# Performance work log

Hardware: AMD Instinct MI355X
Metric: run time of the kernel (lower is better)

## Reference

```python
import jax, jax.numpy as jnp
import numpy as np

N_NODES = 100000
N_EDGES = 250000
N_GRAPHS = 512
VOCAB = 1000
EMBED = 256
HIDDEN = 512
OUT = 128
EPS = 1e-5


def setup_inputs() -> dict:
    key = jax.random.key(0)
    ks = jax.random.split(key, 16)
    s = 0.02
    return {
        "x": jax.random.randint(ks[0], (N_NODES, 1), 0, VOCAB),
        "edge_index": jax.random.randint(ks[1], (2, N_EDGES), 0, N_NODES),
        "batch": jnp.sort(jax.random.randint(ks[2], (N_NODES,), 0, N_GRAPHS)),
        "emb": jax.random.normal(ks[3], (VOCAB, EMBED), jnp.float32) * s,
        "W1": jax.random.normal(ks[4], (EMBED, HIDDEN), jnp.float32) * s,
        "b1": jnp.zeros((HIDDEN,), jnp.float32),
        "g1": jnp.ones((HIDDEN,), jnp.float32),
        "be1": jnp.zeros((HIDDEN,), jnp.float32),
        "W2": jax.random.normal(ks[5], (HIDDEN, HIDDEN), jnp.float32) * s,
        "b2": jnp.zeros((HIDDEN,), jnp.float32),
        "g2": jnp.ones((HIDDEN,), jnp.float32),
        "be2": jnp.zeros((HIDDEN,), jnp.float32),
        "Wl1": jax.random.normal(ks[6], (HIDDEN, HIDDEN // 2), jnp.float32) * s,
        "bl1": jnp.zeros((HIDDEN // 2,), jnp.float32),
        "Wl2": jax.random.normal(ks[7], (HIDDEN // 2, OUT), jnp.float32) * s,
        "bl2": jnp.zeros((OUT,), jnp.float32),
    }


def _mpnn(h, edge_index, W, b):
    # sum-aggregate messages x_j from source to target, plus self-loop, then linear
    src, dst = edge_index[0], edge_index[1]
    agg = jax.ops.segment_sum(h[src], dst, num_segments=h.shape[0]) + h
    return agg @ W + b


def _bn(h, g, be):
    # BatchNorm1d, training-mode batch statistics (biased variance)
    mu = jnp.mean(h, axis=0)
    var = jnp.mean(jnp.square(h - mu), axis=0)
    return (h - mu) * jax.lax.rsqrt(var + EPS) * g + be


def reference(x, edge_index, batch, emb, W1, b1, g1, be1, W2, b2, g2, be2, Wl1, bl1, Wl2, bl2):
    h = emb[x[:, 0]]                                   # [N, EMBED]
    h = jax.nn.relu(_bn(_mpnn(h, edge_index, W1, b1), g1, be1))
    h = jax.nn.relu(_bn(_mpnn(h, edge_index, W2, b2), g2, be2))
    # global mean pool per graph
    sums = jax.ops.segment_sum(h, batch, num_segments=N_GRAPHS)
    cnts = jax.ops.segment_sum(jnp.ones((h.shape[0],), h.dtype), batch, num_segments=N_GRAPHS)
    pooled = sums / jnp.maximum(cnts, 1.0)[:, None]    # [G, HIDDEN]
    z = jax.nn.relu(pooled @ Wl1 + bl1)                # dropout is identity in eval
    return z @ Wl2 + bl2                               # [G, OUT]
```

## Files before the change

kernel.cpp:

```cpp
#include <hip/hip_runtime.h>
#include <cstdint>
#include <cstddef>

#define N_NODES 100000
#define N_EDGES 250000
#define N_GRAPHS 512
#define MTILES 782
#define MPAD (MTILES * 128)
#define SB 256
#define NBLK ((N_NODES + SB - 1) / SB)

using f32x4  = __attribute__((ext_vector_type(4))) float;
using bf16x8 = __attribute__((ext_vector_type(8))) short;

struct alignas(8) U16x4 { unsigned short x, y, z, w; };

__device__ __forceinline__ unsigned short f32_to_bf16(float f) {
    union { float f; uint32_t u; } v; v.f = f;
    uint32_t r = v.u + 0x7FFF + ((v.u >> 16) & 1);
    return (unsigned short)(r >> 16);
}
__device__ __forceinline__ float bf_lo(uint32_t u) {
    union { uint32_t u; float f; } v; v.u = u << 16; return v.f;
}
__device__ __forceinline__ float bf_hi(uint32_t u) {
    union { uint32_t u; float f; } v; v.u = u & 0xFFFF0000u; return v.f;
}

__device__ __forceinline__ void async_cp16(const void* g, void* l) {
    __builtin_amdgcn_global_load_lds(
        (const __attribute__((address_space(1))) void*)g,
        (__attribute__((address_space(3))) void*)l, 16, 0, 0);
}

__global__ void k_zero_int(int* __restrict__ p, int n) {
    int i = blockIdx.x * 256 + threadIdx.x;
    if (i < n) p[i] = 0;
}
__global__ void k_zero_f(float* __restrict__ p, int n) {
    int i = blockIdx.x * 256 + threadIdx.x;
    if (i < n) p[i] = 0.f;
}

__global__ void k_hist(const int* __restrict__ ei, int* __restrict__ counts) {
    int e = blockIdx.x * 256 + threadIdx.x;
    if (e < N_EDGES) atomicAdd(&counts[ei[N_EDGES + e]], 1);
}

__global__ __launch_bounds__(SB) void k_blocksum(const int* __restrict__ counts,
                                                 int* __restrict__ bsum) {
    __shared__ int red[4];
    int i = blockIdx.x * SB + threadIdx.x;
    int v = (i < N_NODES) ? counts[i] : 0;
#pragma unroll
    for (int off = 1; off < 64; off <<= 1) v += __shfl_xor(v, off);
    int wave = threadIdx.x >> 6, lane = threadIdx.x & 63;
    if (lane == 0) red[wave] = v;
    __syncthreads();
    if (threadIdx.x == 0) bsum[blockIdx.x] = red[0] + red[1] + red[2] + red[3];
}

__global__ __launch_bounds__(512) void k_scan_bsum(const int* __restrict__ bsum,
                                                   int* __restrict__ bpre) {
    __shared__ int s[512];
    int t = threadIdx.x;
    int orig = (t < NBLK) ? bsum[t] : 0;
    s[t] = orig;
    __syncthreads();
    for (int off = 1; off < 512; off <<= 1) {
        int v = (t >= off) ? s[t - off] : 0;
        __syncthreads();
        s[t] += v;
        __syncthreads();
    }
    if (t < NBLK) bpre[t] = s[t] - orig;
}

__global__ __launch_bounds__(SB) void k_scan_final(const int* __restrict__ counts,
                                                   const int* __restrict__ bpre,
                                                   int* __restrict__ rowptr,
                                                   int* __restrict__ cursor) {
    __shared__ int s[SB];
    int t = threadIdx.x;
    int i = blockIdx.x * SB + t;
    int c = (i < N_NODES) ? counts[i] : 0;
    s[t] = c;
    __syncthreads();
    for (int off = 1; off < SB; off <<= 1) {
        int v = (t >= off) ? s[t - off] : 0;
        __syncthreads();
        s[t] += v;
        __syncthreads();
    }
    int pre = bpre[blockIdx.x] + s[t] - c;
    if (i < N_NODES) { rowptr[i] = pre; cursor[i] = pre; }
    if (i == 0) rowptr[N_NODES] = N_EDGES;
}

__global__ void k_fill(const int* __restrict__ ei, int* __restrict__ cursor,
                       int* __restrict__ srcs) {
    int e = blockIdx.x * 256 + threadIdx.x;
    if (e < N_EDGES) {
        int dst = ei[N_EDGES + e];
        int p = atomicAdd(&cursor[dst], 1);
        srcs[p] = ei[e];
    }
}

__global__ __launch_bounds__(256) void k_gather1(
    const int* __restrict__ x, const float* __restrict__ emb,
    const int* __restrict__ rowptr, const int* __restrict__ srcs,
    unsigned short* __restrict__ agg1b) {
    int wave = threadIdx.x >> 6, lane = threadIdx.x & 63;
    int node = blockIdx.x * 4 + wave;
    if (node >= N_NODES) return;
    int row = x[node];
    float4 acc = ((const float4*)emb)[(size_t)row * 64 + lane];
    int j0 = rowptr[node], j1 = rowptr[node + 1];
    for (int j = j0; j < j1; ++j) {
        int s = srcs[j];
        int r = x[s];
        float4 v = ((const float4*)emb)[(size_t)r * 64 + lane];
        acc.x += v.x; acc.y += v.y; acc.z += v.z; acc.w += v.w;
    }
    U16x4 o{ f32_to_bf16(acc.x), f32_to_bf16(acc.y), f32_to_bf16(acc.z), f32_to_bf16(acc.w) };
    ((U16x4*)agg1b)[(size_t)node * 64 + lane] = o;
}

#define SLAB_LD 136
template <int K>
__global__ __launch_bounds__(256) void k_gemm_bias_stats(
    const unsigned short* __restrict__ A, const unsigned short* __restrict__ Bt,
    const float* __restrict__ bias, unsigned short* __restrict__ Cb,
    float* __restrict__ colsum, float* __restrict__ colsq, int M) {
    __shared__ __align__(16) unsigned short sh[8192];
    unsigned short* lA = sh;
    unsigned short* lB = sh + 4096;
    const int tid  = threadIdx.x;
    const int wave = tid >> 6, lane = tid & 63;
    const int m0 = blockIdx.y * 128;
    const int n0 = blockIdx.x * 128;
    const int wr = (wave >> 1) * 64;
    const int wc = (wave & 1) * 64;
    const int quad = lane >> 4, m16 = lane & 15;

    f32x4 acc[4][4] = {};

    for (int k0 = 0; k0 < K; k0 += 32) {
        __syncthreads();
#pragma unroll
        for (int t = 0; t < 2; ++t) {
            int seg = (wave * 2 + t) * 64 + lane;
            int row = seg >> 2, cs = seg & 3;
            const unsigned short* gA = A + (size_t)(m0 + row) * K + (k0 + cs * 8);
            async_cp16(gA, &lA[(size_t)((wave * 2 + t) * 64) * 8]);
            const unsigned short* gB = Bt + (size_t)(n0 + row) * K + (k0 + cs * 8);
            async_cp16(gB, &lB[(size_t)((wave * 2 + t) * 64) * 8]);
        }
        __syncthreads();

        bf16x8 af[4], bfr[4];
#pragma unroll
        for (int rb = 0; rb < 4; ++rb)
            af[rb] = *(const bf16x8*)&lA[(wr + rb * 16 + m16) * 32 + quad * 8];
#pragma unroll
        for (int cb = 0; cb < 4; ++cb)
            bfr[cb] = *(const bf16x8*)&lB[(wc + cb * 16 + m16) * 32 + quad * 8];
#pragma unroll
        for (int rb = 0; rb < 4; ++rb)
#pragma unroll
            for (int cb = 0; cb < 4; ++cb)
                acc[rb][cb] = __builtin_amdgcn_mfma_f32_16x16x32_bf16(
                    af[rb], bfr[cb], acc[rb][cb], 0, 0, 0);
    }

    float bvs[4];
#pragma unroll
    for (int cb = 0; cb < 4; ++cb) {
        int col = n0 + wc + cb * 16 + m16;
        float bv = bias[col];
        bvs[cb] = bv;
        float s = 0.f, s2 = 0.f;
#pragma unroll
        for (int rb = 0; rb < 4; ++rb) {
#pragma unroll
            for (int i = 0; i < 4; ++i) {
                int row = m0 + wr + rb * 16 + quad * 4 + i;
                if (row < M) {
                    float v = acc[rb][cb][i] + bv;
                    s += v; s2 += v * v;
                }
            }
        }
        s  += __shfl_xor(s, 16);   s  += __shfl_xor(s, 32);
        s2 += __shfl_xor(s2, 16);  s2 += __shfl_xor(s2, 32);
        if (quad == 0) {
            atomicAdd(&colsum[col], s);
            atomicAdd(&colsq[col], s2);
        }
    }

#pragma unroll
    for (int rb = 0; rb < 4; ++rb) {
        __syncthreads();
#pragma unroll
        for (int cb = 0; cb < 4; ++cb) {
            int scol = wc + cb * 16 + m16;
#pragma unroll
            for (int i = 0; i < 4; ++i) {
                int sr = (wave >> 1) * 16 + quad * 4 + i;
                sh[sr * SLAB_LD + scol] = f32_to_bf16(acc[rb][cb][i] + bvs[cb]);
            }
        }
        __syncthreads();
#pragma unroll
        for (int s = 0; s < 2; ++s) {
            int u = tid + s * 256;
            int sr = u >> 4, c8 = u & 15;
            int gr = m0 + (sr >> 4) * 64 + rb * 16 + (sr & 15);
            uint4 v = *(const uint4*)&sh[sr * SLAB_LD + c8 * 8];
            *(uint4*)&Cb[(size_t)gr * 512 + n0 + c8 * 8] = v;
        }
    }
}

__global__ void k_cvt_wt(const float* __restrict__ W, unsigned short* __restrict__ Wt,
                         int K, int N) {
    int i = blockIdx.x * 256 + threadIdx.x;
    if (i < K * N) {
        int k = i / N, n = i - k * N;
        Wt[(size_t)n * K + k] = f32_to_bf16(W[i]);
    }
}

__global__ void k_bn_coeffs(const float* __restrict__ colsum, const float* __restrict__ colsq,
                            const float* __restrict__ g, const float* __restrict__ be,
                            float* __restrict__ a, float* __restrict__ c) {
    int f = blockIdx.x * 256 + threadIdx.x;
    if (f >= 512) return;
    float mu  = colsum[f] * (1.f / N_NODES);
    float var = colsq[f] * (1.f / N_NODES) - mu * mu;
    float ai  = g[f] * rsqrtf(var + 1e-5f);
    a[f] = ai;
    c[f] = be[f] - mu * ai;
}

__global__ __launch_bounds__(256) void k_gather2(
    const unsigned short* __restrict__ pre1b, const int* __restrict__ rowptr,
    const int* __restrict__ srcs, const float* __restrict__ a1,
    const float* __restrict__ c1, unsigned short* __restrict__ agg2b) {
    int wave = threadIdx.x >> 6, lane = threadIdx.x & 63;
    int node = blockIdx.x * 4 + wave;
    if (node >= N_NODES) return;
    float4 aa0 = ((const float4*)a1)[lane * 2], aa1 = ((const float4*)a1)[lane * 2 + 1];
    float4 cc0 = ((const float4*)c1)[lane * 2], cc1 = ((const float4*)c1)[lane * 2 + 1];
    float acc[8] = {};
    int j0 = rowptr[node], j1 = rowptr[node + 1];
    for (int j = j0 - 1; j < j1; ++j) {
        int s = (j < j0) ? node : srcs[j];
        uint4 raw = ((const uint4*)(pre1b + (size_t)s * 512))[lane];
        acc[0] += fmaxf(fmaf(aa0.x, bf_lo(raw.x), cc0.x), 0.f);
        acc[1] += fmaxf(fmaf(aa0.y, bf_hi(raw.x), cc0.y), 0.f);
        acc[2] += fmaxf(fmaf(aa0.z, bf_lo(raw.y), cc0.z), 0.f);
        acc[3] += fmaxf(fmaf(aa0.w, bf_hi(raw.y), cc0.w), 0.f);
        acc[4] += fmaxf(fmaf(aa1.x, bf_lo(raw.z), cc1.x), 0.f);
        acc[5] += fmaxf(fmaf(aa1.y, bf_hi(raw.z), cc1.y), 0.f);
        acc[6] += fmaxf(fmaf(aa1.z, bf_lo(raw.w), cc1.z), 0.f);
        acc[7] += fmaxf(fmaf(aa1.w, bf_hi(raw.w), cc1.w), 0.f);
    }
    U16x4 o0{ f32_to_bf16(acc[0]), f32_to_bf16(acc[1]), f32_to_bf16(acc[2]), f32_to_bf16(acc[3]) };
    U16x4 o1{ f32_to_bf16(acc[4]), f32_to_bf16(acc[5]), f32_to_bf16(acc[6]), f32_to_bf16(acc[7]) };
    ((U16x4*)agg2b)[(size_t)node * 128 + lane * 2]     = o0;
    ((U16x4*)agg2b)[(size_t)node * 128 + lane * 2 + 1] = o1;
}

__global__ void k_seg_starts(const int* __restrict__ batch, int* __restrict__ starts) {
    int i = blockIdx.x * 256 + threadIdx.x;
    if (i >= N_NODES) return;
    int b = batch[i];
    if (i == 0) {
        for (int g = 0; g <= b; ++g) starts[g] = 0;
    } else {
        int p = batch[i - 1];
        for (int g = p + 1; g <= b; ++g) starts[g] = i;
    }
    if (i == N_NODES - 1) {
        for (int g = b + 1; g <= N_GRAPHS; ++g) starts[g] = N_NODES;
    }
}

__global__ __launch_bounds__(256) void k_pool(const unsigned short* __restrict__ pre2b,
                                              const int* __restrict__ starts,
                                              const float* __restrict__ a2,
                                              const float* __restrict__ c2,
                                              float* __restrict__ pooled) {
    __shared__ float red[3 * 512];
    int g = blockIdx.x;
    int wave = threadIdx.x >> 6, lane = threadIdx.x & 63;
    int s = starts[g], e = starts[g + 1];
    float4 aa0 = ((const float4*)a2)[lane * 2], aa1 = ((const float4*)a2)[lane * 2 + 1];
    float4 cc0 = ((const float4*)c2)[lane * 2], cc1 = ((const float4*)c2)[lane * 2 + 1];
    float acc[8] = {};
    for (int n = s + wave; n < e; n += 4) {
        uint4 raw = ((const uint4*)(pre2b + (size_t)n * 512))[lane];
        acc[0] += fmaxf(fmaf(aa0.x, bf_lo(raw.x), cc0.x), 0.f);
        acc[1] += fmaxf(fmaf(aa0.y, bf_hi(raw.x), cc0.y), 0.f);
        acc[2] += fmaxf(fmaf(aa0.z, bf_lo(raw.y), cc0.z), 0.f);
        acc[3] += fmaxf(fmaf(aa0.w, bf_hi(raw.y), cc0.w), 0.f);
        acc[4] += fmaxf(fmaf(aa1.x, bf_lo(raw.z), cc1.x), 0.f);
        acc[5] += fmaxf(fmaf(aa1.y, bf_hi(raw.z), cc1.y), 0.f);
        acc[6] += fmaxf(fmaf(aa1.z, bf_lo(raw.w), cc1.z), 0.f);
        acc[7] += fmaxf(fmaf(aa1.w, bf_hi(raw.w), cc1.w), 0.f);
    }
    if (wave != 0) {
#pragma unroll
        for (int j = 0; j < 8; ++j) red[(wave - 1) * 512 + lane * 8 + j] = acc[j];
    }
    __syncthreads();
    if (wave == 0) {
#pragma unroll
        for (int j = 0; j < 8; ++j)
            acc[j] += red[lane * 8 + j] + red[512 + lane * 8 + j] + red[1024 + lane * 8 + j];
        float inv = 1.f / fmaxf((float)(e - s), 1.f);
#pragma unroll
        for (int j = 0; j < 8; ++j) pooled[(size_t)g * 512 + lane * 8 + j] = acc[j] * inv;
    }
}

__global__ __launch_bounds__(256) void k_mlp1(const float* __restrict__ pooled,
                                              const float* __restrict__ Wl1,
                                              const float* __restrict__ bl1,
                                              float* __restrict__ z) {
    __shared__ float sp[512];
    int i = blockIdx.x, j = threadIdx.x;
    sp[j]       = pooled[(size_t)i * 512 + j];
    sp[j + 256] = pooled[(size_t)i * 512 + 256 + j];
    __syncthreads();
    float acc = bl1[j];
#pragma unroll 4
    for (int k = 0; k < 512; ++k) acc = fmaf(sp[k], Wl1[(size_t)k * 256 + j], acc);
    z[(size_t)i * 256 + j] = fmaxf(acc, 0.f);
}

__global__ __launch_bounds__(128) void k_mlp2(const float* __restrict__ z,
                                              const float* __restrict__ Wl2,
                                              const float* __restrict__ bl2,
                                              float* __restrict__ out) {
    __shared__ float sz[256];
    int i = blockIdx.x, j = threadIdx.x;
    sz[j]       = z[(size_t)i * 256 + j];
    sz[j + 128] = z[(size_t)i * 256 + 128 + j];
    __syncthreads();
    float acc = bl2[j];
#pragma unroll 4
    for (int k = 0; k < 256; ++k) acc = fmaf(sz[k], Wl2[(size_t)k * 128 + j], acc);
    out[(size_t)i * 128 + j] = acc;
}

extern "C" void kernel_launch(void* const* d_in, const int* in_sizes, int n_in,
                              void* d_out, int out_size, void* d_ws, size_t ws_size,
                              hipStream_t stream) {
    const int*   x    = (const int*)d_in[0];
    const int*   ei   = (const int*)d_in[1];
    const int*   batch= (const int*)d_in[2];
    const float* emb  = (const float*)d_in[3];
    const float* W1   = (const float*)d_in[4];
    const float* b1   = (const float*)d_in[5];
    const float* g1   = (const float*)d_in[6];
    const float* be1  = (const float*)d_in[7];
    const float* W2   = (const float*)d_in[8];
    const float* b2   = (const float*)d_in[9];
    const float* g2   = (const float*)d_in[10];
    const float* be2  = (const float*)d_in[11];
    const float* Wl1  = (const float*)d_in[12];
    const float* bl1  = (const float*)d_in[13];
    const float* Wl2  = (const float*)d_in[14];
    const float* bl2  = (const float*)d_in[15];
    float* out = (float*)d_out;

    char* ws = (char*)d_ws;
    size_t o = 0;
    auto alloc = [&](size_t bytes) { char* p = ws + o; o += (bytes + 255) & ~(size_t)255; return p; };

    unsigned short* W1tb = (unsigned short*)alloc((size_t)512 * 256 * 2);
    unsigned short* W2tb = (unsigned short*)alloc((size_t)512 * 512 * 2);
    float* sums   = (float*)alloc(4 * 512 * 4);
    float* colsum1 = sums, *colsq1 = sums + 512, *colsum2 = sums + 1024, *colsq2 = sums + 1536;
    float* coeffs = (float*)alloc(4 * 512 * 4);
    float* a1 = coeffs, *c1 = coeffs + 512, *a2 = coeffs + 1024, *c2 = coeffs + 1536;
    int*   starts = (int*)alloc((N_GRAPHS + 1) * 4);
    float* pooled = (float*)alloc((size_t)N_GRAPHS * 512 * 4);
    float* zbuf   = (float*)alloc((size_t)N_GRAPHS * 256 * 4);
    int*   counts = (int*)alloc((size_t)N_NODES * 4);
    int*   rowptr = (int*)alloc((size_t)(N_NODES + 1) * 4);
    int*   cursor = (int*)alloc((size_t)N_NODES * 4);
    int*   srcs   = (int*)alloc((size_t)N_EDGES * 4);
    int*   bsum   = (int*)alloc((size_t)NBLK * 4);
    int*   bpre   = (int*)alloc((size_t)NBLK * 4);

    char* slotA = alloc((size_t)MPAD * 512 * 2);
    unsigned short* agg1b = (unsigned short*)slotA;
    unsigned short* agg2b = (unsigned short*)slotA;
    char* slotB = alloc((size_t)MPAD * 512 * 2);
    unsigned short* pre1b = (unsigned short*)slotB;
    unsigned short* pre2b = (unsigned short*)slotB;
    (void)ws_size; (void)in_sizes; (void)n_in; (void)out_size;

    k_zero_int<<<(N_NODES + 255) / 256, 256, 0, stream>>>(counts, N_NODES);
    k_zero_f<<<8, 256, 0, stream>>>(sums, 2048);
    k_hist<<<(N_EDGES + 255) / 256, 256, 0, stream>>>(ei, counts);
    k_blocksum<<<NBLK, SB, 0, stream>>>(counts, bsum);
    k_scan_bsum<<<1, 512, 0, stream>>>(bsum, bpre);
    k_scan_final<<<NBLK, SB, 0, stream>>>(counts, bpre, rowptr, cursor);
    k_fill<<<(N_EDGES + 255) / 256, 256, 0, stream>>>(ei, cursor, srcs);

    k_cvt_wt<<<(256 * 512 + 255) / 256, 256, 0, stream>>>(W1, W1tb, 256, 512);
    k_cvt_wt<<<(512 * 512 + 255) / 256, 256, 0, stream>>>(W2, W2tb, 512, 512);

    k_gather1<<<(N_NODES + 3) / 4, 256, 0, stream>>>(x, emb, rowptr, srcs, agg1b);
    k_gemm_bias_stats<256><<<dim3(4, MTILES), 256, 0, stream>>>(
        agg1b, W1tb, b1, pre1b, colsum1, colsq1, N_NODES);
    k_bn_coeffs<<<2, 256, 0, stream>>>(colsum1, colsq1, g1, be1, a1, c1);

    k_gather2<<<(N_NODES + 3) / 4, 256, 0, stream>>>(pre1b, rowptr, srcs, a1, c1, agg2b);
    k_gemm_bias_stats<512><<<dim3(4, MTILES), 256, 0, stream>>>(
        agg2b, W2tb, b2, pre2b, colsum2, colsq2, N_NODES);
    k_bn_coeffs<<<2, 256, 0, stream>>>(colsum2, colsq2, g2, be2, a2, c2);

    k_seg_starts<<<(N_NODES + 255) / 256, 256, 0, stream>>>(batch, starts);
    k_pool<<<N_GRAPHS, 256, 0, stream>>>(pre2b, starts, a2, c2, pooled);
    k_mlp1<<<N_GRAPHS, 256, 0, stream>>>(pooled, Wl1, bl1, zbuf);
    k_mlp2<<<N_GRAPHS, 128, 0, stream>>>(zbuf, Wl2, bl2, out);
}
```

Before: 524.0 us.

## Double GEMM K-step, swizzle LDS layout, and group tiles for L2 reuse

The GEMM kernel now loads a 64-wide K slab per iteration instead of 32, which halves the barrier count. Shared memory rows are XOR-swizzled to avoid LDS bank conflicts on the fragment reads. The 2D grid becomes a 1D grid remapped so that groups of 8 M-tiles share all 4 N-tiles, meant to improve L2 reuse of A rows. Shared memory per block doubles, which may lower occupancy. Blocks past the last M-tile exit early.

Measured after the change: 477.1 us. -8.9%, faster.

```diff
diff --git a/kernel.cpp b/kernel.cpp
--- a/kernel.cpp
+++ b/kernel.cpp
@@ -9,6 +9,7 @@
 #define MPAD (MTILES * 128)
 #define SB 256
 #define NBLK ((N_NODES + SB - 1) / SB)
+#define GEMM_BLOCKS 3136
 
 using f32x4  = __attribute__((ext_vector_type(4))) float;
 using bf16x8 = __attribute__((ext_vector_type(8))) short;
@@ -133,45 +134,57 @@
     const unsigned short* __restrict__ A, const unsigned short* __restrict__ Bt,
     const float* __restrict__ bias, unsigned short* __restrict__ Cb,
     float* __restrict__ colsum, float* __restrict__ colsq, int M) {
-    __shared__ __align__(16) unsigned short sh[8192];
+    __shared__ __align__(16) unsigned short sh[16384];
     unsigned short* lA = sh;
-    unsigned short* lB = sh + 4096;
+    unsigned short* lB = sh + 8192;
     const int tid  = threadIdx.x;
     const int wave = tid >> 6, lane = tid & 63;
-    const int m0 = blockIdx.y * 128;
-    const int n0 = blockIdx.x * 128;
+    const int b = blockIdx.x;
+    const int m0 = ((b >> 5) * 8 + (b & 7)) * 128;
+    const int n0 = ((b & 31) >> 3) * 128;
+    if (m0 >= M) return;
     const int wr = (wave >> 1) * 64;
     const int wc = (wave & 1) * 64;
     const int quad = lane >> 4, m16 = lane & 15;
 
     f32x4 acc[4][4] = {};
 
-    for (int k0 = 0; k0 < K; k0 += 32) {
-        __syncthreads();
-#pragma unroll
-        for (int t = 0; t < 2; ++t) {
-            int seg = (wave * 2 + t) * 64 + lane;
-            int row = seg >> 2, cs = seg & 3;
+    for (int k0 = 0; k0 < K; k0 += 64) {
+        __syncthreads();
+#pragma unroll
+        for (int t = 0; t < 4; ++t) {
+            int seg = (wave * 4 + t) * 64 + lane;
+            int row = seg >> 3, csl = seg & 7;
+            int cs  = csl ^ (row & 7);
             const unsigned short* gA = A + (size_t)(m0 + row) * K + (k0 + cs * 8);
-            async_cp16(gA, &lA[(size_t)((wave * 2 + t) * 64) * 8]);
+            async_cp16(gA, &lA[seg * 8]);
             const unsigned short* gB = Bt + (size_t)(n0 + row) * K + (k0 + cs * 8);
-            async_cp16(gB, &lB[(size_t)((wave * 2 + t) * 64) * 8]);
-        }
-        __syncthreads();
-
-        bf16x8 af[4], bfr[4];
-#pragma unroll
-        for (int rb = 0; rb < 4; ++rb)
-            af[rb] = *(const bf16x8*)&lA[(wr + rb * 16 + m16) * 32 + quad * 8];
-#pragma unroll
-        for (int cb = 0; cb < 4; ++cb)
-            bfr[cb] = *(const bf16x8*)&lB[(wc + cb * 16 + m16) * 32 + quad * 8];
-#pragma unroll
-        for (int rb = 0; rb < 4; ++rb)
-#pragma unroll
-            for (int cb = 0; cb < 4; ++cb)
-                acc[rb][cb] = __builtin_amdgcn_mfma_f32_16x16x32_bf16(
-                    af[rb], bfr[cb], acc[rb][cb], 0, 0, 0);
+            async_cp16(gB, &lB[seg * 8]);
+        }
+        __syncthreads();
+
+#pragma unroll
+        for (int h = 0; h < 2; ++h) {
+            bf16x8 af[4], bfr[4];
+#pragma unroll
+            for (int rb = 0; rb < 4; ++rb) {
+                int r = wr + rb * 16 + m16;
+                int g = (h * 4 + quad) ^ (r & 7);
+                af[rb] = *(const bf16x8*)&lA[r * 64 + g * 8];
+            }
+#pragma unroll
+            for (int cb = 0; cb < 4; ++cb) {
+                int r = wc + cb * 16 + m16;
+                int g = (h * 4 + quad) ^ (r & 7);
+                bfr[cb] = *(const bf16x8*)&lB[r * 64 + g * 8];
+            }
+#pragma unroll
+            for (int rb = 0; rb < 4; ++rb)
+#pragma unroll
+                for (int cb = 0; cb < 4; ++cb)
+                    acc[rb][cb] = __builtin_amdgcn_mfma_f32_16x16x32_bf16(
+                        af[rb], bfr[cb], acc[rb][cb], 0, 0, 0);
+        }
     }
 
     float bvs[4];
@@ -418,12 +431,12 @@
     k_cvt_wt<<<(512 * 512 + 255) / 256, 256, 0, stream>>>(W2, W2tb, 512, 512);
 
     k_gather1<<<(N_NODES + 3) / 4, 256, 0, stream>>>(x, emb, rowptr, srcs, agg1b);
-    k_gemm_bias_stats<256><<<dim3(4, MTILES), 256, 0, stream>>>(
+    k_gemm_bias_stats<256><<<GEMM_BLOCKS, 256, 0, stream>>>(
         agg1b, W1tb, b1, pre1b, colsum1, colsq1, N_NODES);
     k_bn_coeffs<<<2, 256, 0, stream>>>(colsum1, colsq1, g1, be1, a1, c1);
 
     k_gather2<<<(N_NODES + 3) / 4, 256, 0, stream>>>(pre1b, rowptr, srcs, a1, c1, agg2b);
-    k_gemm_bias_stats<512><<<dim3(4, MTILES), 256, 0, stream>>>(
+    k_gemm_bias_stats<512><<<GEMM_BLOCKS, 256, 0, stream>>>(
         agg2b, W2tb, b2, pre2b, colsum2, colsq2, N_NODES);
     k_bn_coeffs<<<2, 256, 0, stream>>>(colsum2, colsq2, g2, be2, a2, c2);
 
```
